# Kernel tuning notes

Hardware: AMD Instinct MI355X
Metric: run time of the kernel (lower is better)

The kernel has to match this reference:

```python
import jax, jax.numpy as jnp
import numpy as np

N, CIN, COUT, K, STY, H, W = 16, 512, 512, 3, 512, 64, 64
EPS = 1e-8
PAD = K // 2


def setup_inputs() -> dict:
    key = jax.random.key(0)
    k1, k2, k3, k4, k5, k6 = jax.random.split(key, 6)
    x = jax.random.normal(k1, (N, CIN, H, W), dtype=jnp.float32)
    style = jax.random.normal(k2, (N, STY), dtype=jnp.float32)
    noise = jax.random.normal(k3, (N, 1, H, W), dtype=jnp.float32)
    # learned parameters
    weight = jax.random.normal(k4, (1, COUT, CIN, K, K), dtype=jnp.float32)
    style_w = jax.random.normal(k5, (CIN, STY), dtype=jnp.float32) * (1.0 / np.sqrt(STY))
    style_b = jax.random.normal(k6, (CIN,), dtype=jnp.float32) * 0.01 + 1.0  # ~bias_init=1 as in StyleGAN2
    noise_weight = jnp.zeros((1,), dtype=jnp.float32)
    return {"x": x, "style": style, "noise": noise, "weight": weight,
            "style_w": style_w, "style_b": style_b, "noise_weight": noise_weight}


def _per_sample_conv(xi, wi):
    # xi: (CIN, H, W), wi: (COUT, CIN, K, K) -> (COUT, H, W)
    out = jax.lax.conv_general_dilated(
        xi[None], wi, window_strides=(1, 1),
        padding=[(PAD, PAD), (PAD, PAD)],
        dimension_numbers=("NCHW", "OIHW", "NCHW"))
    return out[0]


def reference(x, style, noise, weight, style_w, style_b, noise_weight):
    n = x.shape[0]
    # style modulation: Linear(style_channels -> in_channels), style_bias=0
    s = style @ style_w.T + style_b                     # (N, CIN)
    w = weight * s[:, None, :, None, None]              # (N, COUT, CIN, K, K)
    # demodulation
    demod = jax.lax.rsqrt(jnp.sum(w * w, axis=(2, 3, 4)) + EPS)  # (N, COUT)
    w = w * demod[:, :, None, None, None]
    # grouped conv (groups=batch) == per-sample conv, vmapped over batch
    out = jax.vmap(_per_sample_conv)(x, w)              # (N, COUT, H, W)
    # noise injection + LeakyReLU(0.2)
    out = out + noise_weight[0] * noise
    out = jnp.where(out >= 0, out, 0.2 * out)
    return out
```

## Files before the change

### kernel.cpp

```cpp
#include <hip/hip_runtime.h>
#include <hip/hip_bf16.h>
#include <stdint.h>

#define NB   16
#define CIN  512
#define COUT 512
#define STY  512
#define HH   64
#define WW   64
#define KT   9
#define KDIM (CIN*KT)
#define HP   66
#define PIX  (HH*WW)
#define EPSV 1e-8f

#define SLOT 16384
#define NKT  144

typedef __attribute__((ext_vector_type(8))) __bf16 bf16x8;
typedef __attribute__((ext_vector_type(4))) float floatx4;
typedef unsigned short ushort;

__device__ __forceinline__ ushort f32_to_bf16(float f) {
    union { float f; uint32_t u; } v; v.f = f;
    uint32_t u = v.u;
    u += 0x7fffu + ((u >> 16) & 1u);
    return (ushort)(u >> 16);
}

__device__ __forceinline__ void async16(const void* g, void* l) {
    __builtin_amdgcn_global_load_lds(
        (const __attribute__((address_space(1))) uint32_t*)g,
        (__attribute__((address_space(3))) uint32_t*)l, 16, 0, 0);
}

__global__ void __launch_bounds__(256) style_kernel(
    const float* __restrict__ style, const float* __restrict__ style_w,
    const float* __restrict__ style_b, float* __restrict__ s) {
    const int n = blockIdx.x;
    const int ci = blockIdx.y * 64 + (threadIdx.x >> 2);
    const int q = threadIdx.x & 3;
    const float4* wv = (const float4*)(style_w + (size_t)ci * STY);
    const float4* sv = (const float4*)(style + (size_t)n * STY);
    float acc = 0.f;
    #pragma unroll 8
    for (int j = q; j < STY / 4; j += 4) {
        float4 a = wv[j], b = sv[j];
        acc += a.x * b.x + a.y * b.y + a.z * b.z + a.w * b.w;
    }
    acc += __shfl_down(acc, 2, 4);
    acc += __shfl_down(acc, 1, 4);
    if (q == 0) s[(size_t)n * CIN + ci] = acc + style_b[ci];
}

__global__ void __launch_bounds__(256) modw_kernel(
    const float* __restrict__ weight, const float* __restrict__ s,
    ushort* __restrict__ Wt) {
    __shared__ float wL[KDIM];
    __shared__ float sL[CIN];
    __shared__ float red[4];
    const int co = blockIdx.x, n = blockIdx.y, t = threadIdx.x;
    const float2* wv = (const float2*)(weight + (size_t)co * KDIM);
    float2* wLv = (float2*)wL;
    #pragma unroll
    for (int i = 0; i < 9; ++i) wLv[t + 256 * i] = wv[t + 256 * i];
    ((float2*)sL)[t] = ((const float2*)(s + (size_t)n * CIN))[t];
    __syncthreads();
    float m[18];
    float sum = 0.f;
    #pragma unroll
    for (int c = 0; c < 2; ++c) {
        int ci = 2 * t + c;
        float sm = sL[ci];
        #pragma unroll
        for (int kk = 0; kk < 9; ++kk) {
            float v = wL[ci * 9 + kk] * sm;
            m[c * 9 + kk] = v;
            sum += v * v;
        }
    }
    for (int off = 32; off > 0; off >>= 1) sum += __shfl_down(sum, off, 64);
    if ((t & 63) == 0) red[t >> 6] = sum;
    __syncthreads();
    const float demod = rsqrtf(red[0] + red[1] + red[2] + red[3] + EPSV);
    uint32_t* orow = (uint32_t*)(Wt + (size_t)(n * COUT + co) * KDIM);
    #pragma unroll
    for (int kk = 0; kk < 9; ++kk) {
        uint32_t lo = (uint32_t)f32_to_bf16(m[kk] * demod);
        uint32_t hi = (uint32_t)f32_to_bf16(m[9 + kk] * demod);
        orow[kk * 256 + t] = lo | (hi << 16);
    }
}

__global__ void __launch_bounds__(256) zborder_kernel(unsigned long long* __restrict__ xt8) {
    int idx = blockIdx.x * 256 + threadIdx.x;
    int k = idx & 127;
    int rem = idx >> 7;
    int slot = rem % 260;
    int n = rem / 260;
    int hp, wp;
    if (slot < 66)       { hp = 0;  wp = slot; }
    else if (slot < 132) { hp = 65; wp = slot - 66; }
    else { int r = slot - 132; hp = 1 + (r >> 1); wp = (r & 1) ? 65 : 0; }
    xt8[(size_t)((n * HP + hp) * HP + wp) * 128 + k] = 0ull;
}

__global__ void __launch_bounds__(256) xpose_kernel(
    const float* __restrict__ x, ushort* __restrict__ xt) {
    const int h = blockIdx.x;
    const int n = blockIdx.y;
    const int t = threadIdx.x;
    __shared__ float tile[64][68];
    for (int ci0 = 0; ci0 < CIN; ci0 += 64) {
        #pragma unroll
        for (int r = 0; r < 4; ++r) {
            int cil = r * 16 + (t >> 4);
            int w4 = (t & 15) * 4;
            float4 v = *(const float4*)&x[(((size_t)n * CIN + ci0 + cil) * HH + h) * WW + w4];
            *(float4*)&tile[cil][w4] = v;
        }
        __syncthreads();
        #pragma unroll
        for (int r = 0; r < 8; ++r) {
            int w = (t >> 5) + r * 8;
            int cil = 2 * (t & 31);
            uint32_t lo = (uint32_t)f32_to_bf16(tile[cil][w]);
            uint32_t hi = (uint32_t)f32_to_bf16(tile[cil + 1][w]);
            *(uint32_t*)&xt[(((size_t)n * HP + h + 1) * HP + (w + 1)) * CIN + ci0 + cil] =
                lo | (hi << 16);
        }
        __syncthreads();
    }
}

template<int VMC, bool STAGE>
__device__ __forceinline__ void ktile(
    int kt, short* lds_, const ushort* __restrict__ Wt, const ushort* __restrict__ xt,
    size_t gA0, size_t gA1, size_t gB0, size_t gB1,
    int dA0, int dA1, int dB0, int dB1,
    int aBase, int bBase, floatx4 (&acc)[8][4]) {
    short* sbase = lds_ + (kt & 3) * SLOT;
    __builtin_amdgcn_sched_barrier(0);
    if constexpr (VMC == 8)      asm volatile("s_waitcnt vmcnt(8)" ::: "memory");
    else if constexpr (VMC == 4) asm volatile("s_waitcnt vmcnt(4)" ::: "memory");
    else                         asm volatile("s_waitcnt vmcnt(0)" ::: "memory");
    __builtin_amdgcn_s_barrier();
    __builtin_amdgcn_sched_barrier(0);

    bf16x8 af[4], bv[4];
    #pragma unroll
    for (int i = 0; i < 4; ++i) af[i] = *(const bf16x8*)(sbase + aBase + i * 512);
    #pragma unroll
    for (int i = 0; i < 4; ++i) bv[i] = *(const bf16x8*)(sbase + bBase + i * 512);
    if constexpr (STAGE) {
        short* dbase = lds_ + ((kt + 3) & 3) * SLOT;
        size_t off = (size_t)(kt + 3) * 32;
        async16(Wt + gA0 + off, dbase + dA0);
        async16(Wt + gA1 + off, dbase + dA1);
    }
    __builtin_amdgcn_sched_barrier(0);
    __builtin_amdgcn_s_barrier();
    __builtin_amdgcn_sched_barrier(0);
    __builtin_amdgcn_s_setprio(1);
    #pragma unroll
    for (int mi = 0; mi < 4; ++mi)
        #pragma unroll
        for (int ni = 0; ni < 4; ++ni)
            acc[mi][ni] = __builtin_amdgcn_mfma_f32_16x16x32_bf16(
                af[mi], bv[ni], acc[mi][ni], 0, 0, 0);
    __builtin_amdgcn_s_setprio(0);
    __builtin_amdgcn_sched_barrier(0);
    __builtin_amdgcn_s_barrier();
    __builtin_amdgcn_sched_barrier(0);

    #pragma unroll
    for (int i = 0; i < 4; ++i) af[i] = *(const bf16x8*)(sbase + aBase + 2048 + i * 512);
    if constexpr (STAGE) {
        short* dbase = lds_ + ((kt + 3) & 3) * SLOT;
        int ktp = kt + 3;
        int tap = ktp >> 4;
        int kh = tap / 3, kw = tap - kh * 3;
        size_t off = (size_t)(kh * HP + kw) * CIN + (size_t)((ktp & 15) << 5);
        async16(xt + gB0 + off, dbase + dB0);
        async16(xt + gB1 + off, dbase + dB1);
    }
    __builtin_amdgcn_sched_barrier(0);
    __builtin_amdgcn_s_barrier();
    __builtin_amdgcn_sched_barrier(0);
    __builtin_amdgcn_s_setprio(1);
    #pragma unroll
    for (int mi = 0; mi < 4; ++mi)
        #pragma unroll
        for (int ni = 0; ni < 4; ++ni)
            acc[4 + mi][ni] = __builtin_amdgcn_mfma_f32_16x16x32_bf16(
                af[mi], bv[ni], acc[4 + mi][ni], 0, 0, 0);
    __builtin_amdgcn_s_setprio(0);
    __builtin_amdgcn_sched_barrier(0);
}

__global__ void __launch_bounds__(512, 2) conv_kernel(
    const ushort* __restrict__ Wt, const ushort* __restrict__ xt,
    const float* __restrict__ noise, const float* __restrict__ nw_p,
    float* __restrict__ out) {
    __shared__ short lds[4 * SLOT];
    const int t = threadIdx.x;
    const int bid = blockIdx.x;
    const int xcd = bid & 7;
    const int slot = bid >> 3;
    const int p = slot & 15;
    const int pg = xcd * 4 + (slot >> 4);
    const int n = pg >> 1;
    const int co0 = (pg & 1) * 256;
    const int pos0 = p * 256;
    const int h0 = p * 4;

    const int l = t & 63;
    const int wv = t >> 6;
    const int wr = wv >> 2;
    const int wc = wv & 3;
    const int lrow = l & 15;
    const int lkg = l >> 4;
    const int kcol = (lkg ^ ((l >> 1) & 3)) * 8;
    const int aBase = (wr * 128 + lrow) * 32 + kcol;
    const int bBase = 8192 + (wc * 64 + lrow) * 32 + kcol;

    size_t gAq[2], gBq[2];
    int dAq[2], dBq[2];
    #pragma unroll
    for (int q = 0; q < 2; ++q) {
        int e = q * 4096 + t * 8;
        int row = e >> 5;
        int gr = (e >> 3) & 3;
        int grs = gr ^ ((row >> 1) & 3);
        gAq[q] = (size_t)(n * COUT + co0 + row) * KDIM + grs * 8;
        int prow = row >> 6, pcol = row & 63;
        gBq[q] = ((size_t)(n * HP + h0 + prow) * HP + pcol) * CIN + grs * 8;
        dAq[q] = q * 4096 + t * 8;
        dBq[q] = 8192 + q * 4096 + t * 8;
    }

    floatx4 acc[8][4];
    #pragma unroll
    for (int i = 0; i < 8; ++i)
        #pragma unroll
        for (int j = 0; j < 4; ++j) acc[i][j] = (floatx4){0.f, 0.f, 0.f, 0.f};

    #pragma unroll
    for (int ktp = 0; ktp < 3; ++ktp) {
        short* dbase = lds + ktp * SLOT;
        size_t off = (size_t)ktp * 32;
        async16(Wt + gAq[0] + off, dbase + dAq[0]);
        async16(Wt + gAq[1] + off, dbase + dAq[1]);
        async16(xt + gBq[0] + off, dbase + dBq[0]);
        async16(xt + gBq[1] + off, dbase + dBq[1]);
    }

    #pragma unroll 1
    for (int kt = 0; kt < 141; ++kt)
        ktile<8, true>(kt, lds, Wt, xt, gAq[0], gAq[1], gBq[0], gBq[1],
                       dAq[0], dAq[1], dBq[0], dBq[1], aBase, bBase, acc);
    ktile<8, false>(141, lds, Wt, xt, gAq[0], gAq[1], gBq[0], gBq[1],
                    dAq[0], dAq[1], dBq[0], dBq[1], aBase, bBase, acc);
    ktile<4, false>(142, lds, Wt, xt, gAq[0], gAq[1], gBq[0], gBq[1],
                    dAq[0], dAq[1], dBq[0], dBq[1], aBase, bBase, acc);
    ktile<0, false>(143, lds, Wt, xt, gAq[0], gAq[1], gBq[0], gBq[1],
                    dAq[0], dAq[1], dBq[0], dBq[1], aBase, bBase, acc);

    const float nwv = nw_p[0];
    float nz[4];
    #pragma unroll
    for (int ni = 0; ni < 4; ++ni)
        nz[ni] = nwv * noise[(size_t)n * PIX + pos0 + wc * 64 + ni * 16 + lrow];
    #pragma unroll
    for (int mi = 0; mi < 8; ++mi) {
        #pragma unroll
        for (int r = 0; r < 4; ++r) {
            int cout = co0 + wr * 128 + mi * 16 + lkg * 4 + r;
            float* orow = out + ((size_t)n * COUT + cout) * PIX + pos0 + wc * 64;
            #pragma unroll
            for (int ni = 0; ni < 4; ++ni) {
                float v = acc[mi][ni][r] + nz[ni];
                v = v >= 0.f ? v : 0.2f * v;
                orow[ni * 16 + lrow] = v;
            }
        }
    }
}

extern "C" void kernel_launch(void* const* d_in, const int* in_sizes, int n_in,
                              void* d_out, int out_size, void* d_ws, size_t ws_size,
                              hipStream_t stream) {
    const float* x       = (const float*)d_in[0];
    const float* style   = (const float*)d_in[1];
    const float* noise   = (const float*)d_in[2];
    const float* weight  = (const float*)d_in[3];
    const float* style_w = (const float*)d_in[4];
    const float* style_b = (const float*)d_in[5];
    const float* noise_w = (const float*)d_in[6];
    float* out = (float*)d_out;

    char* ws = (char*)d_ws;
    ushort* Wt = (ushort*)ws;
    ushort* xt = (ushort*)(ws + 75497472);
    float*  s  = (float*)(ws + 75497472 + 71368704);

    hipLaunchKernelGGL(style_kernel,   dim3(16, 8),    dim3(256), 0, stream,
                       style, style_w, style_b, s);
    hipLaunchKernelGGL(modw_kernel,    dim3(512, 16),  dim3(256), 0, stream,
                       weight, s, Wt);
    hipLaunchKernelGGL(zborder_kernel, dim3(2080),     dim3(256), 0, stream,
                       (unsigned long long*)xt);
    hipLaunchKernelGGL(xpose_kernel,   dim3(64, 16),   dim3(256), 0, stream,
                       x, xt);
    hipLaunchKernelGGL(conv_kernel,    dim3(512),      dim3(512), 0, stream,
                       Wt, xt, noise, noise_w, out);
}
```

Before: 524.8 us.

## Merge two per-k-tile MFMA phases into one and drop intra-tile barriers

The per-k-tile body now reads both A halves and B from LDS up front, issues all four async global-to-LDS copies together, and runs all 32 MFMAs in a single phase. This removes three s_barrier/sched_barrier pairs per k-tile, aiming to cut synchronisation stalls. The cost is more live VGPRs for the extra A fragments, which could hurt occupancy at 512 threads x 2 blocks. It also loses the ping-pong interleaving between wave groups that the barriers enforced.

```diff
diff --git a/kernel.cpp b/kernel.cpp
--- a/kernel.cpp
+++ b/kernel.cpp
@@ -147,55 +147,39 @@
     __builtin_amdgcn_s_barrier();
     __builtin_amdgcn_sched_barrier(0);
 
-    bf16x8 af[4], bv[4];
-    #pragma unroll
-    for (int i = 0; i < 4; ++i) af[i] = *(const bf16x8*)(sbase + aBase + i * 512);
+    bf16x8 a0[4], a1[4], bv[4];
+    #pragma unroll
+    for (int i = 0; i < 4; ++i) a0[i] = *(const bf16x8*)(sbase + aBase + i * 512);
     #pragma unroll
     for (int i = 0; i < 4; ++i) bv[i] = *(const bf16x8*)(sbase + bBase + i * 512);
+    #pragma unroll
+    for (int i = 0; i < 4; ++i) a1[i] = *(const bf16x8*)(sbase + aBase + 2048 + i * 512);
     if constexpr (STAGE) {
         short* dbase = lds_ + ((kt + 3) & 3) * SLOT;
-        size_t off = (size_t)(kt + 3) * 32;
-        async16(Wt + gA0 + off, dbase + dA0);
-        async16(Wt + gA1 + off, dbase + dA1);
-    }
-    __builtin_amdgcn_sched_barrier(0);
-    __builtin_amdgcn_s_barrier();
-    __builtin_amdgcn_sched_barrier(0);
-    __builtin_amdgcn_s_setprio(1);
-    #pragma unroll
-    for (int mi = 0; mi < 4; ++mi)
-        #pragma unroll
-        for (int ni = 0; ni < 4; ++ni)
-            acc[mi][ni] = __builtin_amdgcn_mfma_f32_16x16x32_bf16(
-                af[mi], bv[ni], acc[mi][ni], 0, 0, 0);
-    __builtin_amdgcn_s_setprio(0);
-    __builtin_amdgcn_sched_barrier(0);
-    __builtin_amdgcn_s_barrier();
-    __builtin_amdgcn_sched_barrier(0);
-
-    #pragma unroll
-    for (int i = 0; i < 4; ++i) af[i] = *(const bf16x8*)(sbase + aBase + 2048 + i * 512);
-    if constexpr (STAGE) {
-        short* dbase = lds_ + ((kt + 3) & 3) * SLOT;
+        size_t offA = (size_t)(kt + 3) * 32;
+        async16(Wt + gA0 + offA, dbase + dA0);
+        async16(Wt + gA1 + offA, dbase + dA1);
         int ktp = kt + 3;
         int tap = ktp >> 4;
         int kh = tap / 3, kw = tap - kh * 3;
-        size_t off = (size_t)(kh * HP + kw) * CIN + (size_t)((ktp & 15) << 5);
-        async16(xt + gB0 + off, dbase + dB0);
-        async16(xt + gB1 + off, dbase + dB1);
-    }
-    __builtin_amdgcn_sched_barrier(0);
-    __builtin_amdgcn_s_barrier();
-    __builtin_amdgcn_sched_barrier(0);
+        size_t offB = (size_t)(kh * HP + kw) * CIN + (size_t)((ktp & 15) << 5);
+        async16(xt + gB0 + offB, dbase + dB0);
+        async16(xt + gB1 + offB, dbase + dB1);
+    }
     __builtin_amdgcn_s_setprio(1);
+    #pragma unroll
+    for (int mi = 0; mi < 4; ++mi)
+        #pragma unroll
+        for (int ni = 0; ni < 4; ++ni)
+            acc[mi][ni] = __builtin_amdgcn_mfma_f32_16x16x32_bf16(
+                a0[mi], bv[ni], acc[mi][ni], 0, 0, 0);
     #pragma unroll
     for (int mi = 0; mi < 4; ++mi)
         #pragma unroll
         for (int ni = 0; ni < 4; ++ni)
             acc[4 + mi][ni] = __builtin_amdgcn_mfma_f32_16x16x32_bf16(
-                af[mi], bv[ni], acc[4 + mi][ni], 0, 0, 0);
+                a1[mi], bv[ni], acc[4 + mi][ni], 0, 0, 0);
     __builtin_amdgcn_s_setprio(0);
-    __builtin_amdgcn_sched_barrier(0);
 }
 
 __global__ void __launch_bounds__(512, 2) conv_kernel(
```

Result: no change. 530.6 us (+1.1%).
